# Kernel optimization log

Measured on AMD Instinct MI355X. Metric: run time of the kernel, lower is better.

## Reference

```python
import jax, jax.numpy as jnp
import numpy as np

NUM_LAYERS = 3


def setup_inputs() -> dict:
    key = jax.random.key(0)
    k1, k2, k3 = jax.random.split(key, 3)
    N, D, E = 100000, 64, 1250000
    emb = jax.random.normal(k1, (N, D), dtype=jnp.float32)
    edge_attr = jax.random.uniform(k2, (E,), dtype=jnp.float32)
    edge_index = jax.random.randint(k3, (2, E), 0, N, dtype=jnp.int64)
    return {"emb": emb, "edge_attr": edge_attr, "edge_index": edge_index}


def reference(emb, edge_attr, edge_index):
    # LightGCN.get_embedding with uniform alpha = 1/(num_layers+1)
    N = emb.shape[0]
    src, dst = edge_index[0], edge_index[1]
    # gcn_norm (add_self_loops=False): symmetric normalization of edge weights
    deg = jax.ops.segment_sum(edge_attr, dst, num_segments=N)  # [N]
    dinv = jnp.where(deg > 0, jax.lax.rsqrt(deg), 0.0)
    w = dinv[src] * edge_attr * dinv[dst]  # [E]
    alpha = jnp.float32(1.0 / (NUM_LAYERS + 1))
    x = emb
    out = x * alpha
    for _ in range(NUM_LAYERS):
        # gather source embeddings, scale by normalized weight, scatter-add to dst
        msgs = x[src] * w[:, None]  # [E, D]
        x = jax.ops.segment_sum(msgs, dst, num_segments=N)  # [N, D]
        out = out + x * alpha
    return out
```

## Files before the change

kernel.cpp:

```cpp
#include <hip/hip_runtime.h>
#include <hip/hip_fp16.h>


#define G 256
#define SH 6
#define BNODES 64
#define WINV (1.0f / 32767.0f)

typedef float f4_native __attribute__((ext_vector_type(4)));

__global__ void __launch_bounds__(256) k_bhist(const int* __restrict__ ei,
                                               int* __restrict__ bcnt, int NB, int E) {
    extern __shared__ unsigned int hist[];
    int g = blockIdx.x, t = threadIdx.x;
    for (int b = t; b < NB; b += 256) hist[b] = 0;
    __syncthreads();
    int chunk = (E + G - 1) / G;
    int lo = g * chunk;
    int hi = min(lo + chunk, E);
    for (int i = lo + t; i < hi; i += 256) {
        int d = ei[E + i];
        atomicAdd(&hist[d >> SH], 1u);
    }
    __syncthreads();
    for (int b = t; b < NB; b += 256) bcnt[(size_t)g * NB + b] = (int)hist[b];
}

__global__ void k_colprefix(const int* __restrict__ bcnt, int* __restrict__ sc0,
                            int* __restrict__ btot, int NB) {
    int b = blockIdx.x * blockDim.x + threadIdx.x;
    if (b >= NB) return;
    int run = 0;
    #pragma unroll 8
    for (int g = 0; g < G; ++g) {
        int v = bcnt[(size_t)g * NB + b];
        sc0[(size_t)g * NB + b] = run;
        run += v;
    }
    btot[b] = run;
}

__global__ void __launch_bounds__(256) k_btot_scan(const int* __restrict__ btot,
                                                   int* __restrict__ bbase, int NB) {
    __shared__ int s[256];
    __shared__ int carry;
    int t = threadIdx.x;
    if (t == 0) carry = 0;
    __syncthreads();
    int ntile = (NB + 255) / 256;
    for (int tile = 0; tile < ntile; ++tile) {
        int i = tile * 256 + t;
        int v = (i < NB) ? btot[i] : 0;
        s[t] = v;
        __syncthreads();
        for (int off = 1; off < 256; off <<= 1) {
            int x = (t >= off) ? s[t - off] : 0;
            __syncthreads();
            s[t] += x;
            __syncthreads();
        }
        int incl = s[t];
        int c = carry;
        if (i < NB) bbase[i] = c + incl - v;
        __syncthreads();
        if (t == 255) carry = c + incl;
        __syncthreads();
    }
    if (t == 0) bbase[NB] = carry;
}

__global__ void __launch_bounds__(256) k_bscatter(const int* __restrict__ ei,
                                                  const float* __restrict__ ea,
                                                  const int* __restrict__ sc0,
                                                  const int* __restrict__ bbase,
                                                  int2* __restrict__ ebuf, int NB, int E) {
    extern __shared__ unsigned int cur[];
    int g = blockIdx.x, t = threadIdx.x;
    for (int b = t; b < NB; b += 256)
        cur[b] = (unsigned)(bbase[b] + sc0[(size_t)g * NB + b]);
    __syncthreads();
    int chunk = (E + G - 1) / G;
    int lo = g * chunk;
    int hi = min(lo + chunk, E);
    for (int i = lo + t; i < hi; i += 256) {
        int srcv = ei[i];
        int d = ei[E + i];
        float w = ea[i];
        unsigned pos = atomicAdd(&cur[d >> SH], 1u);
        int2 m;
        m.x = srcv | ((d & (BNODES - 1)) << 25);
        m.y = __float_as_int(w);
        ebuf[pos] = m;
    }
}

__global__ void __launch_bounds__(256) k_bfinal(const int2* __restrict__ ebuf,
                                                const int* __restrict__ bbase,
                                                const float2* __restrict__ emb2,
                                                unsigned int* __restrict__ meta,
                                                int* __restrict__ row_start,
                                                float* __restrict__ dinv,
                                                __half2* __restrict__ z0,
                                                int NB, int N, int E) {
    __shared__ unsigned int hcnt[BNODES];
    __shared__ float hsum[BNODES];
    __shared__ unsigned int hoff[BNODES];
    __shared__ unsigned int cur[BNODES];
    __shared__ float sdv[BNODES];
    int b = blockIdx.x, t = threadIdx.x;
    if (t < BNODES) {
        hcnt[t] = 0;
        hsum[t] = 0.0f;
    }
    __syncthreads();
    int e0 = bbase[b];
    int e1 = bbase[b + 1];
    for (int i = e0 + t; i < e1; i += 256) {
        int2 m = ebuf[i];
        int dl = (m.x >> 25) & (BNODES - 1);
        atomicAdd(&hcnt[dl], 1u);
        atomicAdd(&hsum[dl], __int_as_float(m.y));
    }
    __syncthreads();
    if (t == 0) {
        unsigned r = 0;
        for (int k = 0; k < BNODES; ++k) {
            hoff[k] = r;
            r += hcnt[k];
        }
    }
    __syncthreads();
    if (t < BNODES) {
        cur[t] = hoff[t];
        float s = hsum[t];
        float dv = (s > 0.0f) ? rsqrtf(s) : 0.0f;
        sdv[t] = dv;
        int node = (b << SH) + t;
        if (node < N) {
            row_start[node] = e0 + (int)hoff[t];
            dinv[node] = dv;
        }
    }
    if (b == 0 && t == 0) row_start[N] = E;
    __syncthreads();
    for (int i = e0 + t; i < e1; i += 256) {
        int2 m = ebuf[i];
        int dl = (m.x >> 25) & (BNODES - 1);
        unsigned p = atomicAdd(&cur[dl], 1u);
        float w = __int_as_float(m.y);
        unsigned q = (unsigned)__float2int_rn(w * 32767.0f);
        q = min(q, 32767u);
        meta[e0 + (int)p] = (unsigned)(m.x & ((1 << 17) - 1)) | (q << 17);
    }
    int base = b << SH;
    for (int idx = t; idx < BNODES * 32; idx += 256) {
        int node = idx >> 5;
        int gnode = base + node;
        if (gnode < N) {
            float s = sdv[node];
            float2 v = emb2[(size_t)gnode * 32 + (idx & 31)];
            z0[(size_t)gnode * 32 + (idx & 31)] = __floats2half2_rn(v.x * s, v.y * s);
        }
    }
}

union F2H {
    float2 f;
    __half2 h[2];
};

template <int MODE>
__global__ void __launch_bounds__(256) k_prop(const float2* __restrict__ zin,
                                              const unsigned int* __restrict__ meta,
                                              const int* __restrict__ row_start,
                                              const float* __restrict__ dinv,
                                              float2* __restrict__ zout,
                                              const float4* __restrict__ emb,
                                              const float2* __restrict__ z1,
                                              const float2* __restrict__ z2,
                                              float4* __restrict__ out, int N) {
    int g = (blockIdx.x * 256 + threadIdx.x) >> 4;
    if (g >= N) return;
    int l = threadIdx.x & 15;
    int b = row_start[g];
    int e = row_start[g + 1];

    float4 acc = make_float4(0.f, 0.f, 0.f, 0.f);
    int i = b;
    for (; i + 8 <= e; i += 8) {
        unsigned mm[8];
        F2H uu[8];
        #pragma unroll
        for (int k = 0; k < 8; ++k) mm[k] = meta[i + k];
        #pragma unroll
        for (int k = 0; k < 8; ++k) uu[k].f = zin[(size_t)(mm[k] & 0x1FFFFu) * 16 + l];
        #pragma unroll
        for (int k = 0; k < 8; ++k) {
            float w = (float)(mm[k] >> 17) * WINV;
            float2 a = __half22float2(uu[k].h[0]), bb = __half22float2(uu[k].h[1]);
            acc.x = fmaf(a.x, w, acc.x);
            acc.y = fmaf(a.y, w, acc.y);
            acc.z = fmaf(bb.x, w, acc.z);
            acc.w = fmaf(bb.y, w, acc.w);
        }
    }
    for (; i + 4 <= e; i += 4) {
        unsigned mm[4];
        F2H uu[4];
        #pragma unroll
        for (int k = 0; k < 4; ++k) mm[k] = meta[i + k];
        #pragma unroll
        for (int k = 0; k < 4; ++k) uu[k].f = zin[(size_t)(mm[k] & 0x1FFFFu) * 16 + l];
        #pragma unroll
        for (int k = 0; k < 4; ++k) {
            float w = (float)(mm[k] >> 17) * WINV;
            float2 a = __half22float2(uu[k].h[0]), bb = __half22float2(uu[k].h[1]);
            acc.x = fmaf(a.x, w, acc.x);
            acc.y = fmaf(a.y, w, acc.y);
            acc.z = fmaf(bb.x, w, acc.z);
            acc.w = fmaf(bb.y, w, acc.w);
        }
    }
    for (; i < e; ++i) {
        unsigned m = meta[i];
        F2H u;
        u.f = zin[(size_t)(m & 0x1FFFFu) * 16 + l];
        float w = (float)(m >> 17) * WINV;
        float2 a = __half22float2(u.h[0]), bb = __half22float2(u.h[1]);
        acc.x = fmaf(a.x, w, acc.x);
        acc.y = fmaf(a.y, w, acc.y);
        acc.z = fmaf(bb.x, w, acc.z);
        acc.w = fmaf(bb.y, w, acc.w);
    }

    float sd = dinv[g];
    int o = g * 16 + l;
    if (MODE == 0) {
        float s2 = sd * sd;
        F2H u;
        u.h[0] = __floats2half2_rn(s2 * acc.x, s2 * acc.y);
        u.h[1] = __floats2half2_rn(s2 * acc.z, s2 * acc.w);
        zout[o] = u.f;
    } else {
        float rd = (sd > 0.0f) ? (1.0f / sd) : 0.0f;
        F2H u1, u2;
        u1.f = z1[o];
        u2.f = z2[o];
        float2 a1 = __half22float2(u1.h[0]), b1 = __half22float2(u1.h[1]);
        float2 a2 = __half22float2(u2.h[0]), b2 = __half22float2(u2.h[1]);
        float4 ev = emb[o];
        f4_native r;
        r.x = 0.25f * (ev.x + rd * (a1.x + a2.x) + sd * acc.x);
        r.y = 0.25f * (ev.y + rd * (a1.y + a2.y) + sd * acc.y);
        r.z = 0.25f * (ev.z + rd * (b1.x + b2.x) + sd * acc.z);
        r.w = 0.25f * (ev.w + rd * (b1.y + b2.y) + sd * acc.w);
        __builtin_nontemporal_store(r, reinterpret_cast<f4_native*>(&out[o]));
    }
}

static inline size_t align_up(size_t x, size_t a) { return (x + a - 1) & ~(a - 1); }

extern "C" void kernel_launch(void* const* d_in, const int* in_sizes, int n_in,
                              void* d_out, int out_size, void* d_ws, size_t ws_size,
                              hipStream_t stream) {
    const float* emb = (const float*)d_in[0];
    const float* ea  = (const float*)d_in[1];
    const int*   ei  = (const int*)d_in[2];
    float* out = (float*)d_out;

    const int D = 64;
    const int N = in_sizes[0] / D;
    const int E = in_sizes[1];

    const int NB = (N + BNODES - 1) / BNODES;
    const int NS = NB * G;

    char* ws = (char*)d_ws;
    size_t off = 0;
    int* bcnt = (int*)(ws + off);           off = align_up(off + (size_t)NS * 4, 256);
    int* sc0 = (int*)(ws + off);            off = align_up(off + (size_t)NS * 4, 256);
    int* btot = (int*)(ws + off);           off = align_up(off + (size_t)NB * 4, 256);
    int* bbase = (int*)(ws + off);          off = align_up(off + (size_t)(NB + 1) * 4, 256);
    int* row_start = (int*)(ws + off);      off = align_up(off + (size_t)(N + 1) * 4, 256);
    float* dinv = (float*)(ws + off);       off = align_up(off + (size_t)N * 4, 256);
    int2* ebuf = (int2*)(ws + off);         off = align_up(off + (size_t)E * 8, 256);
    unsigned int* meta = (unsigned int*)(ws + off); off = align_up(off + (size_t)E * 4, 256);
    __half2* z0 = (__half2*)(ws + off);     off = align_up(off + (size_t)N * D * 2, 256);
    __half2* z1 = (__half2*)(ws + off);     off = align_up(off + (size_t)N * D * 2, 256);
    __half2* z2 = (__half2*)(ws + off);     off = align_up(off + (size_t)N * D * 2, 256);
    (void)ws_size;

    k_bhist<<<G, 256, NB * 4, stream>>>(ei, bcnt, NB, E);
    k_colprefix<<<(NB + 255) / 256, 256, 0, stream>>>(bcnt, sc0, btot, NB);
    k_btot_scan<<<1, 256, 0, stream>>>(btot, bbase, NB);
    k_bscatter<<<G, 256, NB * 4, stream>>>(ei, ea, sc0, bbase, ebuf, NB, E);
    k_bfinal<<<NB, 256, 0, stream>>>(ebuf, bbase, (const float2*)emb, meta, row_start,
                                     dinv, z0, NB, N, E);

    int lb = (N * 16 + 255) / 256;
    k_prop<0><<<lb, 256, 0, stream>>>((const float2*)z0, meta, row_start, dinv,
                                      (float2*)z1, nullptr, nullptr, nullptr, nullptr, N);
    k_prop<0><<<lb, 256, 0, stream>>>((const float2*)z1, meta, row_start, dinv,
                                      (float2*)z2, nullptr, nullptr, nullptr, nullptr, N);
    k_prop<1><<<lb, 256, 0, stream>>>((const float2*)z2, meta, row_start, dinv,
                                      nullptr, (const float4*)emb, (const float2*)z1,
                                      (const float2*)z2, (float4*)out, N);
}
```

Measured before the change: 155.1 us.

## Widen buckets to 512 nodes and replace prefix-scan kernels with atomic chunk bases

```diff
diff --git a/kernel.cpp b/kernel.cpp
--- a/kernel.cpp
+++ b/kernel.cpp
@@ -3,14 +3,14 @@
 
 
 #define G 256
-#define SH 6
-#define BNODES 64
+#define SH 9
+#define BNODES 512
 #define WINV (1.0f / 32767.0f)
 
-typedef float f4_native __attribute__((ext_vector_type(4)));
-
-__global__ void __launch_bounds__(256) k_bhist(const int* __restrict__ ei,
-                                               int* __restrict__ bcnt, int NB, int E) {
+__global__ void __launch_bounds__(256) k_hist(const int* __restrict__ ei,
+                                              unsigned int* __restrict__ gcur,
+                                              int* __restrict__ chunkbase,
+                                              int NB, int E) {
     extern __shared__ unsigned int hist[];
     int g = blockIdx.x, t = threadIdx.x;
     for (int b = t; b < NB; b += 256) hist[b] = 0;
@@ -23,61 +23,31 @@
         atomicAdd(&hist[d >> SH], 1u);
     }
     __syncthreads();
-    for (int b = t; b < NB; b += 256) bcnt[(size_t)g * NB + b] = (int)hist[b];
-}
-
-__global__ void k_colprefix(const int* __restrict__ bcnt, int* __restrict__ sc0,
-                            int* __restrict__ btot, int NB) {
-    int b = blockIdx.x * blockDim.x + threadIdx.x;
-    if (b >= NB) return;
-    int run = 0;
-    #pragma unroll 8
-    for (int g = 0; g < G; ++g) {
-        int v = bcnt[(size_t)g * NB + b];
-        sc0[(size_t)g * NB + b] = run;
-        run += v;
-    }
-    btot[b] = run;
-}
-
-__global__ void __launch_bounds__(256) k_btot_scan(const int* __restrict__ btot,
-                                                   int* __restrict__ bbase, int NB) {
-    __shared__ int s[256];
-    __shared__ int carry;
-    int t = threadIdx.x;
-    if (t == 0) carry = 0;
-    __syncthreads();
-    int ntile = (NB + 255) / 256;
-    for (int tile = 0; tile < ntile; ++tile) {
-        int i = tile * 256 + t;
-        int v = (i < NB) ? btot[i] : 0;
-        s[t] = v;
-        __syncthreads();
-        for (int off = 1; off < 256; off <<= 1) {
-            int x = (t >= off) ? s[t - off] : 0;
-            __syncthreads();
-            s[t] += x;
-            __syncthreads();
-        }
-        int incl = s[t];
-        int c = carry;
-        if (i < NB) bbase[i] = c + incl - v;
-        __syncthreads();
-        if (t == 255) carry = c + incl;
-        __syncthreads();
-    }
-    if (t == 0) bbase[NB] = carry;
+    for (int b = t; b < NB; b += 256) {
+        unsigned h = hist[b];
+        unsigned base = atomicAdd(&gcur[b], h);
+        chunkbase[(size_t)g * NB + b] = (int)base;
+    }
 }
 
 __global__ void __launch_bounds__(256) k_bscatter(const int* __restrict__ ei,
                                                   const float* __restrict__ ea,
-                                                  const int* __restrict__ sc0,
-                                                  const int* __restrict__ bbase,
+                                                  const unsigned int* __restrict__ gcur,
+                                                  const int* __restrict__ chunkbase,
                                                   int2* __restrict__ ebuf, int NB, int E) {
     extern __shared__ unsigned int cur[];
+    __shared__ int tot[256];
     int g = blockIdx.x, t = threadIdx.x;
+    tot[t] = (t < NB) ? (int)gcur[t] : 0;
+    __syncthreads();
+    for (int off = 1; off < 256; off <<= 1) {
+        int x = (t >= off) ? tot[t - off] : 0;
+        __syncthreads();
+        tot[t] += x;
+        __syncthreads();
+    }
     for (int b = t; b < NB; b += 256)
-        cur[b] = (unsigned)(bbase[b] + sc0[(size_t)g * NB + b]);
+        cur[b] = (unsigned)(tot[b] - (int)gcur[b] + chunkbase[(size_t)g * NB + b]);
     __syncthreads();
     int chunk = (E + G - 1) / G;
     int lo = g * chunk;
@@ -88,64 +58,72 @@
         float w = ea[i];
         unsigned pos = atomicAdd(&cur[d >> SH], 1u);
         int2 m;
-        m.x = srcv | ((d & (BNODES - 1)) << 25);
+        m.x = srcv | ((d & (BNODES - 1)) << 17);
         m.y = __float_as_int(w);
         ebuf[pos] = m;
     }
 }
 
-__global__ void __launch_bounds__(256) k_bfinal(const int2* __restrict__ ebuf,
-                                                const int* __restrict__ bbase,
+__global__ void __launch_bounds__(512) k_bfinal(const int2* __restrict__ ebuf,
+                                                const unsigned int* __restrict__ gcur,
                                                 const float2* __restrict__ emb2,
                                                 unsigned int* __restrict__ meta,
                                                 int* __restrict__ row_start,
                                                 float* __restrict__ dinv,
                                                 __half2* __restrict__ z0,
                                                 int NB, int N, int E) {
+    __shared__ int tot[256];
     __shared__ unsigned int hcnt[BNODES];
     __shared__ float hsum[BNODES];
-    __shared__ unsigned int hoff[BNODES];
+    __shared__ int sbuf[BNODES];
     __shared__ unsigned int cur[BNODES];
     __shared__ float sdv[BNODES];
     int b = blockIdx.x, t = threadIdx.x;
-    if (t < BNODES) {
-        hcnt[t] = 0;
-        hsum[t] = 0.0f;
-    }
-    __syncthreads();
-    int e0 = bbase[b];
-    int e1 = bbase[b + 1];
-    for (int i = e0 + t; i < e1; i += 256) {
+
+    if (t < 256) tot[t] = (t < NB) ? (int)gcur[t] : 0;
+    __syncthreads();
+    for (int off = 1; off < 256; off <<= 1) {
+        int x = (t < 256 && t >= off) ? tot[t - off] : 0;
+        __syncthreads();
+        if (t < 256) tot[t] += x;
+        __syncthreads();
+    }
+    int e1 = tot[b];
+    int e0 = e1 - (int)gcur[b];
+
+    hcnt[t] = 0;
+    hsum[t] = 0.0f;
+    __syncthreads();
+    for (int i = e0 + t; i < e1; i += 512) {
         int2 m = ebuf[i];
-        int dl = (m.x >> 25) & (BNODES - 1);
+        int dl = (m.x >> 17) & (BNODES - 1);
         atomicAdd(&hcnt[dl], 1u);
         atomicAdd(&hsum[dl], __int_as_float(m.y));
     }
     __syncthreads();
-    if (t == 0) {
-        unsigned r = 0;
-        for (int k = 0; k < BNODES; ++k) {
-            hoff[k] = r;
-            r += hcnt[k];
-        }
-    }
-    __syncthreads();
-    if (t < BNODES) {
-        cur[t] = hoff[t];
-        float s = hsum[t];
-        float dv = (s > 0.0f) ? rsqrtf(s) : 0.0f;
-        sdv[t] = dv;
-        int node = (b << SH) + t;
-        if (node < N) {
-            row_start[node] = e0 + (int)hoff[t];
-            dinv[node] = dv;
-        }
+    sbuf[t] = (int)hcnt[t];
+    __syncthreads();
+    for (int off = 1; off < BNODES; off <<= 1) {
+        int x = (t >= off) ? sbuf[t - off] : 0;
+        __syncthreads();
+        sbuf[t] += x;
+        __syncthreads();
+    }
+    int excl = sbuf[t] - (int)hcnt[t];
+    cur[t] = (unsigned)excl;
+    float s = hsum[t];
+    float dv = (s > 0.0f) ? rsqrtf(s) : 0.0f;
+    sdv[t] = dv;
+    int node = (b << SH) + t;
+    if (node < N) {
+        row_start[node] = e0 + excl;
+        dinv[node] = dv;
     }
     if (b == 0 && t == 0) row_start[N] = E;
     __syncthreads();
-    for (int i = e0 + t; i < e1; i += 256) {
+    for (int i = e0 + t; i < e1; i += 512) {
         int2 m = ebuf[i];
-        int dl = (m.x >> 25) & (BNODES - 1);
+        int dl = (m.x >> 17) & (BNODES - 1);
         unsigned p = atomicAdd(&cur[dl], 1u);
         float w = __int_as_float(m.y);
         unsigned q = (unsigned)__float2int_rn(w * 32767.0f);
@@ -153,13 +131,13 @@
         meta[e0 + (int)p] = (unsigned)(m.x & ((1 << 17) - 1)) | (q << 17);
     }
     int base = b << SH;
-    for (int idx = t; idx < BNODES * 32; idx += 256) {
-        int node = idx >> 5;
-        int gnode = base + node;
+    for (int idx = t; idx < BNODES * 32; idx += 512) {
+        int nd = idx >> 5;
+        int gnode = base + nd;
         if (gnode < N) {
-            float s = sdv[node];
+            float sc = sdv[nd];
             float2 v = emb2[(size_t)gnode * 32 + (idx & 31)];
-            z0[(size_t)gnode * 32 + (idx & 31)] = __floats2half2_rn(v.x * s, v.y * s);
+            z0[(size_t)gnode * 32 + (idx & 31)] = __floats2half2_rn(v.x * sc, v.y * sc);
         }
     }
 }
@@ -249,12 +227,12 @@
         float2 a1 = __half22float2(u1.h[0]), b1 = __half22float2(u1.h[1]);
         float2 a2 = __half22float2(u2.h[0]), b2 = __half22float2(u2.h[1]);
         float4 ev = emb[o];
-        f4_native r;
+        float4 r;
         r.x = 0.25f * (ev.x + rd * (a1.x + a2.x) + sd * acc.x);
         r.y = 0.25f * (ev.y + rd * (a1.y + a2.y) + sd * acc.y);
         r.z = 0.25f * (ev.z + rd * (b1.x + b2.x) + sd * acc.z);
         r.w = 0.25f * (ev.w + rd * (b1.y + b2.y) + sd * acc.w);
-        __builtin_nontemporal_store(r, reinterpret_cast<f4_native*>(&out[o]));
+        out[o] = r;
     }
 }
 
@@ -273,14 +251,12 @@
     const int E = in_sizes[1];
 
     const int NB = (N + BNODES - 1) / BNODES;
-    const int NS = NB * G;
 
     char* ws = (char*)d_ws;
     size_t off = 0;
-    int* bcnt = (int*)(ws + off);           off = align_up(off + (size_t)NS * 4, 256);
-    int* sc0 = (int*)(ws + off);            off = align_up(off + (size_t)NS * 4, 256);
-    int* btot = (int*)(ws + off);           off = align_up(off + (size_t)NB * 4, 256);
-    int* bbase = (int*)(ws + off);          off = align_up(off + (size_t)(NB + 1) * 4, 256);
+    unsigned int* gcur = (unsigned int*)(ws + off);
+                                            off = align_up(off + (size_t)NB * 4, 256);
+    int* chunkbase = (int*)(ws + off);      off = align_up(off + (size_t)G * NB * 4, 256);
     int* row_start = (int*)(ws + off);      off = align_up(off + (size_t)(N + 1) * 4, 256);
     float* dinv = (float*)(ws + off);       off = align_up(off + (size_t)N * 4, 256);
     int2* ebuf = (int2*)(ws + off);         off = align_up(off + (size_t)E * 8, 256);
@@ -290,11 +266,10 @@
     __half2* z2 = (__half2*)(ws + off);     off = align_up(off + (size_t)N * D * 2, 256);
     (void)ws_size;
 
-    k_bhist<<<G, 256, NB * 4, stream>>>(ei, bcnt, NB, E);
-    k_colprefix<<<(NB + 255) / 256, 256, 0, stream>>>(bcnt, sc0, btot, NB);
-    k_btot_scan<<<1, 256, 0, stream>>>(btot, bbase, NB);
-    k_bscatter<<<G, 256, NB * 4, stream>>>(ei, ea, sc0, bbase, ebuf, NB, E);
-    k_bfinal<<<NB, 256, 0, stream>>>(ebuf, bbase, (const float2*)emb, meta, row_start,
+    hipMemsetAsync(gcur, 0, (size_t)NB * 4, stream);
+    k_hist<<<G, 256, NB * 4, stream>>>(ei, gcur, chunkbase, NB, E);
+    k_bscatter<<<G, 256, NB * 4, stream>>>(ei, ea, gcur, chunkbase, ebuf, NB, E);
+    k_bfinal<<<NB, 512, 0, stream>>>(ebuf, gcur, (const float2*)emb, meta, row_start,
                                      dinv, z0, NB, N, E);
 
     int lb = (N * 16 + 255) / 256;
```

Result: faster. 147.8 us (-4.7%).
